# Kernel optimization log

Measured on AMD Instinct MI355X. Metric: run time of the kernel, lower is better.

Reference implementation:

```python
import jax, jax.numpy as jnp
from jax import lax
import numpy as np

B, SQ, SK, H, NH, KS = 2, 2048, 2048, 1024, 16, 3
D = H // NH  # depth per head = 64


def setup_inputs() -> dict:
    key = jax.random.key(0)
    ks = jax.random.split(key, 10)
    s = 0.02
    return {
        "query_input": jax.random.normal(ks[0], (B, SQ, H), jnp.float32),
        "source_input": jax.random.normal(ks[1], (B, SK, H), jnp.float32),
        "mask": jnp.zeros((B, 1, 1, SK), jnp.float32),
        "Wq": jax.random.normal(ks[2], (KS, H, H), jnp.float32) * s,
        "bq": jnp.zeros((H,), jnp.float32),
        "Wk": jax.random.normal(ks[3], (KS, H, H), jnp.float32) * s,
        "bk": jnp.zeros((H,), jnp.float32),
        "Wv": jax.random.normal(ks[4], (KS, H, H), jnp.float32) * s,
        "bv": jnp.zeros((H,), jnp.float32),
        "Wo": jax.random.normal(ks[5], (H, H), jnp.float32) * s,
        "bo": jnp.zeros((H,), jnp.float32),
    }


def _conv1d_same(x, W, b):
    # x: [B, S, H], W: [KS, H_in, H_out] -> 'same' padded 1D conv
    y = lax.conv_general_dilated(x, W, window_strides=(1,), padding="SAME",
                                 dimension_numbers=("NWC", "WIO", "NWC"))
    return y + b


def _split_heads(x):
    # [B, S, H] -> [B, NH, S, D]
    b, s, _ = x.shape
    return x.reshape(b, s, NH, D).transpose(0, 2, 1, 3)


def reference(query_input, source_input, mask, Wq, bq, Wk, bk, Wv, bv, Wo, bo):
    q = _split_heads(_conv1d_same(query_input, Wq, bq)) * (D ** -0.5)
    k = _split_heads(_conv1d_same(source_input, Wk, bk))
    v = _split_heads(_conv1d_same(source_input, Wv, bv))
    logits = jnp.einsum("bhqd,bhkd->bhqk", q, k) + mask * (-1e9)
    weights = jax.nn.softmax(logits, axis=-1)  # dropout omitted (eval mode)
    attn = jnp.einsum("bhqk,bhkd->bhqd", weights, v)
    attn = attn.transpose(0, 2, 1, 3).reshape(q.shape[0], -1, H)
    return attn @ Wo + bo
```

## Files before the change

kernel.cpp:

```cpp
#include <hip/hip_runtime.h>
#include <stdint.h>

#define B_   2
#define S_   2048
#define H_   1024
#define NH_  16
#define D_   64
#define KC_  3072

typedef __attribute__((ext_vector_type(8))) short  short8;
typedef __attribute__((ext_vector_type(4))) float  floatx4;

typedef __attribute__((address_space(1))) const void gas_void;
typedef __attribute__((address_space(3))) void       las_void;

__device__ __forceinline__ void gld16(const void* g, void* l) {
    __builtin_amdgcn_global_load_lds((gas_void*)g, (las_void*)l, 16, 0, 0);
}

__device__ __forceinline__ unsigned short f2bf(float f) {
    union { float f; unsigned u; } v; v.f = f;
    unsigned r = v.u + 0x7fffu + ((v.u >> 16) & 1u);
    return (unsigned short)(r >> 16);
}

__global__ __launch_bounds__(256) void k_pad_convert(const float* __restrict__ src,
                                                     unsigned short* __restrict__ dst) {
    int gid = blockIdx.x * 256 + threadIdx.x;
    int vid = gid * 4;
    if (vid >= B_ * 2050 * 1024) return;
    int row = vid >> 10;
    int b   = (row >= 2050) ? 1 : 0;
    int r   = row - b * 2050;
    int h   = vid & 1023;
    unsigned short o0 = 0, o1 = 0, o2 = 0, o3 = 0;
    if (r != 0 && r != 2049) {
        const float4 f = *(const float4*)(src + ((b * 2048 + r - 1) << 10) + h);
        o0 = f2bf(f.x); o1 = f2bf(f.y); o2 = f2bf(f.z); o3 = f2bf(f.w);
    }
    ushort4 o; o.x = o0; o.y = o1; o.z = o2; o.w = o3;
    *(ushort4*)(dst + vid) = o;
}

__global__ void k_transpose_bf16(const float* __restrict__ src,
                                 unsigned short* __restrict__ dst, int R, int C) {
    __shared__ float t[32][33];
    int c0 = blockIdx.x * 32, r0 = blockIdx.y * 32;
    int tx = threadIdx.x, ty = threadIdx.y;
#pragma unroll
    for (int k = 0; k < 4; ++k)
        t[ty + k * 8][tx] = src[(long)(r0 + ty + k * 8) * C + c0 + tx];
    __syncthreads();
#pragma unroll
    for (int k = 0; k < 4; ++k)
        dst[(long)(c0 + ty + k * 8) * R + r0 + tx] = f2bf(t[tx][ty + k * 8]);
}

__global__ __launch_bounds__(256) void k_conv_gemm(
    const unsigned short* __restrict__ xq, const unsigned short* __restrict__ xs,
    const unsigned short* __restrict__ Wqt, const unsigned short* __restrict__ Wkt,
    const unsigned short* __restrict__ Wvt,
    const float* __restrict__ bq, const float* __restrict__ bk, const float* __restrict__ bv,
    unsigned short* __restrict__ Qo, unsigned short* __restrict__ Ko,
    unsigned short* __restrict__ Vo) {
    int z = blockIdx.z;
    const unsigned short* X = (z == 0) ? xq : xs;
    const unsigned short* W = (z == 0) ? Wqt : (z == 1 ? Wkt : Wvt);
    const float* bias = (z == 0) ? bq : (z == 1 ? bk : bv);

    __shared__ unsigned short Al[128 * 64];
    __shared__ unsigned short Bl[128 * 64];

    int n0 = blockIdx.x * 128, m0 = blockIdx.y * 128;
    int b = m0 >> 11;
    int tid = threadIdx.x, lane = tid & 63, w = tid >> 6;
    int quad = lane >> 4, l15 = lane & 15;
    int wm = w >> 1, wn = w & 1;

    floatx4 acc[4][4];
#pragma unroll
    for (int i = 0; i < 4; ++i)
#pragma unroll
        for (int j = 0; j < 4; ++j) acc[i][j] = (floatx4){0.f, 0.f, 0.f, 0.f};

    int arow0 = (m0 + 2 * b) * 1024;

    for (int k0 = 0; k0 < KC_; k0 += 64) {
#pragma unroll
        for (int it = 0; it < 4; ++it) {
            int e  = (it * 256 + tid) * 8;
            int rl = e >> 6;
            int cp = (e >> 3) & 7;
            int c  = cp ^ (rl & 7);
            gld16(X + arow0 + rl * 1024 + k0 + c * 8, (char*)Al + e * 2);
            gld16(W + (n0 + rl) * KC_ + k0 + c * 8, (char*)Bl + e * 2);
        }
        __syncthreads();
#pragma unroll
        for (int kk = 0; kk < 2; ++kk) {
            short8 af[4], bf[4];
#pragma unroll
            for (int i = 0; i < 4; ++i) {
                int m  = wm * 64 + i * 16 + l15;
                int cp = (kk * 4 + quad) ^ (m & 7);
                af[i]  = *(const short8*)(Al + m * 64 + cp * 8);
            }
#pragma unroll
            for (int j = 0; j < 4; ++j) {
                int n  = wn * 64 + j * 16 + l15;
                int cp = (kk * 4 + quad) ^ (n & 7);
                bf[j]  = *(const short8*)(Bl + n * 64 + cp * 8);
            }
#pragma unroll
            for (int i = 0; i < 4; ++i)
#pragma unroll
                for (int j = 0; j < 4; ++j)
                    acc[i][j] = __builtin_amdgcn_mfma_f32_16x16x32_bf16(af[i], bf[j], acc[i][j], 0, 0, 0);
        }
        __syncthreads();
    }

#pragma unroll
    for (int j = 0; j < 4; ++j) {
        int n = n0 + wn * 64 + j * 16 + l15;
        float bb = bias[n];
        int nh = n >> 6, d = n & 63;
#pragma unroll
        for (int i = 0; i < 4; ++i) {
            int srow = (m0 & 2047) + wm * 64 + i * 16 + quad * 4;
#pragma unroll
            for (int r = 0; r < 4; ++r) {
                float v = acc[i][j][r] + bb;
                int s = srow + r;
                if (z == 0)
                    Qo[((b * NH_ + nh) * 2048 + s) * 64 + d] = f2bf(v * 0.125f);
                else if (z == 1)
                    Ko[((b * NH_ + nh) * 2048 + s) * 64 + d] = f2bf(v);
                else
                    Vo[((b * NH_ + nh) * 64 + d) * 2048 + s] = f2bf(v);
            }
        }
    }
}

__global__ __launch_bounds__(256) void k_flash(
    const unsigned short* __restrict__ Q, const unsigned short* __restrict__ K,
    const unsigned short* __restrict__ Vt, const float* __restrict__ mask,
    unsigned short* __restrict__ Ao) {
    __shared__ unsigned short Ul[128 * 136];
    __shared__ unsigned short Vl[64 * 128];

    int tid = threadIdx.x, w = tid >> 6, lane = tid & 63;
    int quad = lane >> 4, l15 = lane & 15;
    int bh = blockIdx.y;
    int b = bh >> 4, nh = bh & 15;
    int q0 = blockIdx.x * 128, wq = w * 32;

    short8 qf[2][2];
#pragma unroll
    for (int i = 0; i < 2; ++i)
#pragma unroll
        for (int kk = 0; kk < 2; ++kk)
            qf[i][kk] = *(const short8*)(Q + ((bh * 2048 + q0 + wq + i * 16 + l15) << 6) + kk * 32 + quad * 8);

    floatx4 oacc[2][4];
    float rsum[2][4];
#pragma unroll
    for (int i = 0; i < 2; ++i) {
#pragma unroll
        for (int j = 0; j < 4; ++j) oacc[i][j] = (floatx4){0.f, 0.f, 0.f, 0.f};
#pragma unroll
        for (int r = 0; r < 4; ++r) rsum[i][r] = 0.f;
    }
    const float* maskb = mask + b * S_;

    for (int kt = 0; kt < 16; ++kt) {
        int k0 = kt * 128;
#pragma unroll
        for (int it = 0; it < 4; ++it) {
            int e  = (it * 256 + tid) * 8;
            int kl = e >> 6;
            int c  = ((e >> 3) & 7) ^ (kl & 7);
            gld16(K + (bh * 2048 + k0 + kl) * 64 + c * 8, (char*)Ul + e * 2);
            int dl = e >> 7;
            int cp = (e >> 3) & 15;
            int c2 = (cp & 8) | ((cp ^ dl) & 7);
            gld16(Vt + (bh * 64 + dl) * 2048 + k0 + c2 * 8, (char*)Vl + e * 2);
        }
        __syncthreads();

        floatx4 sacc[2][8];
#pragma unroll
        for (int i = 0; i < 2; ++i)
#pragma unroll
            for (int j = 0; j < 8; ++j) sacc[i][j] = (floatx4){0.f, 0.f, 0.f, 0.f};
#pragma unroll
        for (int j = 0; j < 8; ++j) {
            int kl = j * 16 + l15;
            short8 bf0, bf1;
            {
                int cp = (0 * 4 + quad) ^ (kl & 7);
                bf0 = *(const short8*)(Ul + kl * 64 + cp * 8);
                int cq = (1 * 4 + quad) ^ (kl & 7);
                bf1 = *(const short8*)(Ul + kl * 64 + cq * 8);
            }
#pragma unroll
            for (int i = 0; i < 2; ++i) {
                sacc[i][j] = __builtin_amdgcn_mfma_f32_16x16x32_bf16(qf[i][0], bf0, sacc[i][j], 0, 0, 0);
                sacc[i][j] = __builtin_amdgcn_mfma_f32_16x16x32_bf16(qf[i][1], bf1, sacc[i][j], 0, 0, 0);
            }
        }
        __syncthreads();

#pragma unroll
        for (int j = 0; j < 8; ++j) {
            float mv = maskb[k0 + j * 16 + l15] * (-1e9f);
#pragma unroll
            for (int i = 0; i < 2; ++i) {
                int row = wq + i * 16 + quad * 4;
#pragma unroll
                for (int r = 0; r < 4; ++r) {
                    float p = __expf(sacc[i][j][r] + mv);
                    rsum[i][r] += p;
                    Ul[(row + r) * 136 + j * 16 + l15] = f2bf(p);
                }
            }
        }

#pragma unroll
        for (int kk = 0; kk < 4; ++kk) {
            short8 af[2], bv4[4];
#pragma unroll
            for (int i = 0; i < 2; ++i)
                af[i] = *(const short8*)(Ul + (wq + i * 16 + l15) * 136 + kk * 32 + quad * 8);
#pragma unroll
            for (int j2 = 0; j2 < 4; ++j2) {
                int dl = j2 * 16 + l15;
                int c  = kk * 4 + quad;
                int cp = (c & 8) | ((c ^ dl) & 7);
                bv4[j2] = *(const short8*)(Vl + dl * 128 + cp * 8);
            }
#pragma unroll
            for (int i = 0; i < 2; ++i)
#pragma unroll
                for (int j2 = 0; j2 < 4; ++j2)
                    oacc[i][j2] = __builtin_amdgcn_mfma_f32_16x16x32_bf16(af[i], bv4[j2], oacc[i][j2], 0, 0, 0);
        }
        __syncthreads();
    }

#pragma unroll
    for (int i = 0; i < 2; ++i)
#pragma unroll
        for (int r = 0; r < 4; ++r) {
            float v = rsum[i][r];
            v += __shfl_xor(v, 1); v += __shfl_xor(v, 2);
            v += __shfl_xor(v, 4); v += __shfl_xor(v, 8);
            rsum[i][r] = 1.0f / v;
        }

#pragma unroll
    for (int i = 0; i < 2; ++i)
#pragma unroll
        for (int j2 = 0; j2 < 4; ++j2)
#pragma unroll
            for (int r = 0; r < 4; ++r) {
                int qrow = q0 + wq + i * 16 + quad * 4 + r;
                int hcol = nh * 64 + j2 * 16 + l15;
                Ao[(b * 2048 + qrow) * 1024 + hcol] = f2bf(oacc[i][j2][r] * rsum[i][r]);
            }
}

__global__ __launch_bounds__(256) void k_proj_gemm(
    const unsigned short* __restrict__ A, const unsigned short* __restrict__ Wt,
    const float* __restrict__ bo, float* __restrict__ out) {
    __shared__ unsigned short Al[128 * 64];
    __shared__ unsigned short Bl[128 * 64];

    int n0 = blockIdx.x * 128, m0 = blockIdx.y * 128;
    int tid = threadIdx.x, lane = tid & 63, w = tid >> 6;
    int quad = lane >> 4, l15 = lane & 15;
    int wm = w >> 1, wn = w & 1;

    floatx4 acc[4][4];
#pragma unroll
    for (int i = 0; i < 4; ++i)
#pragma unroll
        for (int j = 0; j < 4; ++j) acc[i][j] = (floatx4){0.f, 0.f, 0.f, 0.f};

    for (int k0 = 0; k0 < 1024; k0 += 64) {
#pragma unroll
        for (int it = 0; it < 4; ++it) {
            int e  = (it * 256 + tid) * 8;
            int rl = e >> 6;
            int cp = (e >> 3) & 7;
            int c  = cp ^ (rl & 7);
            gld16(A + (m0 + rl) * 1024 + k0 + c * 8, (char*)Al + e * 2);
            gld16(Wt + (n0 + rl) * 1024 + k0 + c * 8, (char*)Bl + e * 2);
        }
        __syncthreads();
#pragma unroll
        for (int kk = 0; kk < 2; ++kk) {
            short8 af[4], bf[4];
#pragma unroll
            for (int i = 0; i < 4; ++i) {
                int m  = wm * 64 + i * 16 + l15;
                int cp = (kk * 4 + quad) ^ (m & 7);
                af[i]  = *(const short8*)(Al + m * 64 + cp * 8);
            }
#pragma unroll
            for (int j = 0; j < 4; ++j) {
                int n  = wn * 64 + j * 16 + l15;
                int cp = (kk * 4 + quad) ^ (n & 7);
                bf[j]  = *(const short8*)(Bl + n * 64 + cp * 8);
            }
#pragma unroll
            for (int i = 0; i < 4; ++i)
#pragma unroll
                for (int j = 0; j < 4; ++j)
                    acc[i][j] = __builtin_amdgcn_mfma_f32_16x16x32_bf16(af[i], bf[j], acc[i][j], 0, 0, 0);
        }
        __syncthreads();
    }

#pragma unroll
    for (int j = 0; j < 4; ++j) {
        int n = n0 + wn * 64 + j * 16 + l15;
        float bb = bo[n];
#pragma unroll
        for (int i = 0; i < 4; ++i) {
            int m = m0 + wm * 64 + i * 16 + quad * 4;
#pragma unroll
            for (int r = 0; r < 4; ++r)
                out[(m + r) * 1024 + n] = acc[i][j][r] + bb;
        }
    }
}

extern "C" void kernel_launch(void* const* d_in, const int* in_sizes, int n_in,
                              void* d_out, int out_size, void* d_ws, size_t ws_size,
                              hipStream_t stream) {
    (void)in_sizes; (void)n_in; (void)out_size; (void)ws_size;
    const float* q_in = (const float*)d_in[0];
    const float* s_in = (const float*)d_in[1];
    const float* mask = (const float*)d_in[2];
    const float* Wq   = (const float*)d_in[3];
    const float* bq   = (const float*)d_in[4];
    const float* Wk   = (const float*)d_in[5];
    const float* bk   = (const float*)d_in[6];
    const float* Wv   = (const float*)d_in[7];
    const float* bv   = (const float*)d_in[8];
    const float* Wo   = (const float*)d_in[9];
    const float* bo   = (const float*)d_in[10];
    float* out = (float*)d_out;

    char* ws = (char*)d_ws;
    size_t off = 0;
    auto alloc = [&](size_t bytes) {
        char* p = ws + off;
        off += (bytes + 255) & ~(size_t)255;
        return p;
    };
    unsigned short* xqp = (unsigned short*)alloc((size_t)B_ * 2050 * 1024 * 2);
    unsigned short* xsp = (unsigned short*)alloc((size_t)B_ * 2050 * 1024 * 2);
    unsigned short* Wqt = (unsigned short*)alloc((size_t)KC_ * H_ * 2);
    unsigned short* Wkt = (unsigned short*)alloc((size_t)KC_ * H_ * 2);
    unsigned short* Wvt = (unsigned short*)alloc((size_t)KC_ * H_ * 2);
    unsigned short* Wot = (unsigned short*)alloc((size_t)H_ * H_ * 2);
    unsigned short* Qb  = (unsigned short*)alloc((size_t)B_ * NH_ * S_ * D_ * 2);
    unsigned short* Kb  = (unsigned short*)alloc((size_t)B_ * NH_ * S_ * D_ * 2);
    unsigned short* Vtb = (unsigned short*)alloc((size_t)B_ * NH_ * S_ * D_ * 2);
    unsigned short* Ab  = (unsigned short*)alloc((size_t)B_ * S_ * H_ * 2);

    k_pad_convert<<<4100, 256, 0, stream>>>(q_in, xqp);
    k_pad_convert<<<4100, 256, 0, stream>>>(s_in, xsp);
    k_transpose_bf16<<<dim3(32, 96), dim3(32, 8), 0, stream>>>(Wq, Wqt, KC_, H_);
    k_transpose_bf16<<<dim3(32, 96), dim3(32, 8), 0, stream>>>(Wk, Wkt, KC_, H_);
    k_transpose_bf16<<<dim3(32, 96), dim3(32, 8), 0, stream>>>(Wv, Wvt, KC_, H_);
    k_transpose_bf16<<<dim3(32, 32), dim3(32, 8), 0, stream>>>(Wo, Wot, H_, H_);
    k_conv_gemm<<<dim3(8, 32, 3), 256, 0, stream>>>(xqp, xsp, Wqt, Wkt, Wvt,
                                                    bq, bk, bv, Qb, Kb, Vtb);
    k_flash<<<dim3(16, 32), 256, 0, stream>>>(Qb, Kb, Vtb, mask, Ab);
    k_proj_gemm<<<dim3(8, 32), 256, 0, stream>>>(Ab, Wot, bo, out);
}
```

Baseline: 358.1 us.

## Double-buffer LDS tiles in conv and projection GEMMs to overlap loads with MFMA

Both GEMM kernels now use two LDS buffers per operand, issuing the global-to-LDS loads for the next K tile before computing on the current one. Address offsets are precomputed once outside the loop, and the loop runs two tiles per iteration with one barrier per tile instead of two. The aim is to hide global load latency behind matrix work. In exchange LDS use per block doubles to 64 KB, which may cut occupancy. The attention kernel edit only moves some declarations around.

Result: no change. 361.3 us (+0.9%).

```diff
diff --git a/kernel.cpp b/kernel.cpp
--- a/kernel.cpp
+++ b/kernel.cpp
@@ -68,8 +68,8 @@
     const unsigned short* W = (z == 0) ? Wqt : (z == 1 ? Wkt : Wvt);
     const float* bias = (z == 0) ? bq : (z == 1 ? bk : bv);
 
-    __shared__ unsigned short Al[128 * 64];
-    __shared__ unsigned short Bl[128 * 64];
+    __shared__ unsigned short Al[2][128 * 64];
+    __shared__ unsigned short Bl[2][128 * 64];
 
     int n0 = blockIdx.x * 128, m0 = blockIdx.y * 128;
     int b = m0 >> 11;
@@ -85,17 +85,26 @@
 
     int arow0 = (m0 + 2 * b) * 1024;
 
-    for (int k0 = 0; k0 < KC_; k0 += 64) {
+    int eoff[4], aoff[4], boff[4];
+#pragma unroll
+    for (int it = 0; it < 4; ++it) {
+        int e  = (it * 256 + tid) * 8;
+        int rl = e >> 6;
+        int cp = (e >> 3) & 7;
+        int c  = cp ^ (rl & 7);
+        eoff[it] = e;
+        aoff[it] = arow0 + rl * 1024 + c * 8;
+        boff[it] = (n0 + rl) * KC_ + c * 8;
+    }
+
+    auto stage = [&](int buf, int k0) {
 #pragma unroll
         for (int it = 0; it < 4; ++it) {
-            int e  = (it * 256 + tid) * 8;
-            int rl = e >> 6;
-            int cp = (e >> 3) & 7;
-            int c  = cp ^ (rl & 7);
-            gld16(X + arow0 + rl * 1024 + k0 + c * 8, (char*)Al + e * 2);
-            gld16(W + (n0 + rl) * KC_ + k0 + c * 8, (char*)Bl + e * 2);
-        }
-        __syncthreads();
+            gld16(X + aoff[it] + k0, (char*)Al[buf] + eoff[it] * 2);
+            gld16(W + boff[it] + k0, (char*)Bl[buf] + eoff[it] * 2);
+        }
+    };
+    auto compute = [&](int buf) {
 #pragma unroll
         for (int kk = 0; kk < 2; ++kk) {
             short8 af[4], bf[4];
@@ -103,13 +112,13 @@
             for (int i = 0; i < 4; ++i) {
                 int m  = wm * 64 + i * 16 + l15;
                 int cp = (kk * 4 + quad) ^ (m & 7);
-                af[i]  = *(const short8*)(Al + m * 64 + cp * 8);
+                af[i]  = *(const short8*)(Al[buf] + m * 64 + cp * 8);
             }
 #pragma unroll
             for (int j = 0; j < 4; ++j) {
                 int n  = wn * 64 + j * 16 + l15;
                 int cp = (kk * 4 + quad) ^ (n & 7);
-                bf[j]  = *(const short8*)(Bl + n * 64 + cp * 8);
+                bf[j]  = *(const short8*)(Bl[buf] + n * 64 + cp * 8);
             }
 #pragma unroll
             for (int i = 0; i < 4; ++i)
@@ -117,6 +126,16 @@
                 for (int j = 0; j < 4; ++j)
                     acc[i][j] = __builtin_amdgcn_mfma_f32_16x16x32_bf16(af[i], bf[j], acc[i][j], 0, 0, 0);
         }
+    };
+
+    stage(0, 0);
+    __syncthreads();
+    for (int kt = 0; kt < 48; kt += 2) {
+        if (kt + 1 < 48) stage(1, (kt + 1) * 64);
+        compute(0);
+        __syncthreads();
+        if (kt + 2 < 48) stage(0, (kt + 2) * 64);
+        compute(1);
         __syncthreads();
     }
 
@@ -197,13 +216,10 @@
 #pragma unroll
         for (int j = 0; j < 8; ++j) {
             int kl = j * 16 + l15;
-            short8 bf0, bf1;
-            {
-                int cp = (0 * 4 + quad) ^ (kl & 7);
-                bf0 = *(const short8*)(Ul + kl * 64 + cp * 8);
-                int cq = (1 * 4 + quad) ^ (kl & 7);
-                bf1 = *(const short8*)(Ul + kl * 64 + cq * 8);
-            }
+            int cp0 = (0 * 4 + quad) ^ (kl & 7);
+            short8 bf0 = *(const short8*)(Ul + kl * 64 + cp0 * 8);
+            int cp1 = (1 * 4 + quad) ^ (kl & 7);
+            short8 bf1 = *(const short8*)(Ul + kl * 64 + cp1 * 8);
 #pragma unroll
             for (int i = 0; i < 2; ++i) {
                 sacc[i][j] = __builtin_amdgcn_mfma_f32_16x16x32_bf16(qf[i][0], bf0, sacc[i][j], 0, 0, 0);
@@ -274,8 +290,8 @@
 __global__ __launch_bounds__(256) void k_proj_gemm(
     const unsigned short* __restrict__ A, const unsigned short* __restrict__ Wt,
     const float* __restrict__ bo, float* __restrict__ out) {
-    __shared__ unsigned short Al[128 * 64];
-    __shared__ unsigned short Bl[128 * 64];
+    __shared__ unsigned short Al[2][128 * 64];
+    __shared__ unsigned short Bl[2][128 * 64];
 
     int n0 = blockIdx.x * 128, m0 = blockIdx.y * 128;
     int tid = threadIdx.x, lane = tid & 63, w = tid >> 6;
@@ -288,17 +304,25 @@
 #pragma unroll
         for (int j = 0; j < 4; ++j) acc[i][j] = (floatx4){0.f, 0.f, 0.f, 0.f};
 
-    for (int k0 = 0; k0 < 1024; k0 += 64) {
+    int eoff[4], aoff[4], boff[4];
+#pragma unroll
+    for (int it = 0; it < 4; ++it) {
+        int e  = (it * 256 + tid) * 8;
+        int rl = e >> 6;
+        int c  = ((e >> 3) & 7) ^ (rl & 7);
+        eoff[it] = e;
+        aoff[it] = (m0 + rl) * 1024 + c * 8;
+        boff[it] = (n0 + rl) * 1024 + c * 8;
+    }
+
+    auto stage = [&](int buf, int k0) {
 #pragma unroll
         for (int it = 0; it < 4; ++it) {
-            int e  = (it * 256 + tid) * 8;
-            int rl = e >> 6;
-            int cp = (e >> 3) & 7;
-            int c  = cp ^ (rl & 7);
-            gld16(A + (m0 + rl) * 1024 + k0 + c * 8, (char*)Al + e * 2);
-            gld16(Wt + (n0 + rl) * 1024 + k0 + c * 8, (char*)Bl + e * 2);
-        }
-        __syncthreads();
+            gld16(A + aoff[it] + k0, (char*)Al[buf] + eoff[it] * 2);
+            gld16(Wt + boff[it] + k0, (char*)Bl[buf] + eoff[it] * 2);
+        }
+    };
+    auto compute = [&](int buf) {
 #pragma unroll
         for (int kk = 0; kk < 2; ++kk) {
             short8 af[4], bf[4];
@@ -306,13 +330,13 @@
             for (int i = 0; i < 4; ++i) {
                 int m  = wm * 64 + i * 16 + l15;
                 int cp = (kk * 4 + quad) ^ (m & 7);
-                af[i]  = *(const short8*)(Al + m * 64 + cp * 8);
+                af[i]  = *(const short8*)(Al[buf] + m * 64 + cp * 8);
             }
 #pragma unroll
             for (int j = 0; j < 4; ++j) {
                 int n  = wn * 64 + j * 16 + l15;
                 int cp = (kk * 4 + quad) ^ (n & 7);
-                bf[j]  = *(const short8*)(Bl + n * 64 + cp * 8);
+                bf[j]  = *(const short8*)(Bl[buf] + n * 64 + cp * 8);
             }
 #pragma unroll
             for (int i = 0; i < 4; ++i)
@@ -320,6 +344,16 @@
                 for (int j = 0; j < 4; ++j)
                     acc[i][j] = __builtin_amdgcn_mfma_f32_16x16x32_bf16(af[i], bf[j], acc[i][j], 0, 0, 0);
         }
+    };
+
+    stage(0, 0);
+    __syncthreads();
+    for (int kt = 0; kt < 16; kt += 2) {
+        if (kt + 1 < 16) stage(1, (kt + 1) * 64);
+        compute(0);
+        __syncthreads();
+        if (kt + 2 < 16) stage(0, (kt + 2) * 64);
+        compute(1);
         __syncthreads();
     }
 
```
